# Optimization experiments

Measured on AMD Instinct MI355X. Metric: run time of the kernel, lower is better.

## Reference

```python
import jax, jax.numpy as jnp
import numpy as np

F = 128; K = 64; SR_CUT = 10.0
NB = 5; NRI = 3; NRA = 2; NRO = 1
N_ATOMS = 10000; N_PAIRS = 320000


def act(x):
    # shifted softplus: softplus(x) - log(2)
    return jax.nn.softplus(x) - jnp.log(2.0).astype(x.dtype)


def residual(x, W1, b1, W2, b2):
    # PhysNet residual: x + dense2(dense1(act(x))) with activation on dense1
    h = act(act(x) @ W1 + b1)
    return x + h @ W2 + b2


def cutoff_fn(D):
    x = D / SR_CUT
    x3 = x * x * x; x4 = x3 * x; x5 = x4 * x
    return jnp.where(x < 1.0, 1.0 - 6.0 * x5 + 15.0 * x4 - 10.0 * x3, 0.0)


def setup_inputs() -> dict:
    key = jax.random.key(0)
    ks = jax.random.split(key, 24)

    def nrm(k, shape, s=0.05):
        return (jax.random.normal(k, shape) * s).astype(jnp.float32)

    inp = {}
    inp["Z"] = jax.random.randint(ks[0], (N_ATOMS,), 1, 95)
    inp["R"] = (jax.random.normal(ks[1], (N_ATOMS, 3)) * 3.0).astype(jnp.float32)
    inp["idx_i"] = jax.random.randint(ks[2], (N_PAIRS,), 0, N_ATOMS)
    inp["idx_j"] = jax.random.randint(ks[3], (N_PAIRS,), 0, N_ATOMS)
    s3 = float(np.sqrt(3.0))
    inp["embeddings"] = jax.random.uniform(ks[4], (95, F), minval=-s3, maxval=s3).astype(jnp.float32)
    inp["rbf_centers"] = jnp.linspace(1.0, float(np.exp(-SR_CUT)), K).astype(jnp.float32)
    width = (0.5 / ((1.0 - float(np.exp(-SR_CUT))) / K)) ** 2
    inp["rbf_widths"] = jnp.full((K,), width, dtype=jnp.float32)
    inp["k2f_W"] = nrm(ks[5], (NB, K, F))
    inp["Wi"] = nrm(ks[6], (NB, F, F)); inp["bi"] = jnp.zeros((NB, F), jnp.float32)
    inp["Wj"] = nrm(ks[7], (NB, F, F)); inp["bj"] = jnp.zeros((NB, F), jnp.float32)
    inp["ri_W1"] = nrm(ks[8], (NB, NRI, F, F)); inp["ri_b1"] = jnp.zeros((NB, NRI, F), jnp.float32)
    inp["ri_W2"] = nrm(ks[9], (NB, NRI, F, F)); inp["ri_b2"] = jnp.zeros((NB, NRI, F), jnp.float32)
    inp["dW"] = nrm(ks[10], (NB, F, F)); inp["db"] = jnp.zeros((NB, F), jnp.float32)
    inp["u"] = jnp.ones((NB, F), jnp.float32)
    inp["ra_W1"] = nrm(ks[11], (NB, NRA, F, F)); inp["ra_b1"] = jnp.zeros((NB, NRA, F), jnp.float32)
    inp["ra_W2"] = nrm(ks[12], (NB, NRA, F, F)); inp["ra_b2"] = jnp.zeros((NB, NRA, F), jnp.float32)
    inp["ro_W1"] = nrm(ks[13], (NB, NRO, F, F)); inp["ro_b1"] = jnp.zeros((NB, NRO, F), jnp.float32)
    inp["ro_W2"] = nrm(ks[14], (NB, NRO, F, F)); inp["ro_b2"] = jnp.zeros((NB, NRO, F), jnp.float32)
    inp["out_W"] = nrm(ks[15], (NB, F, 2))
    inp["Escale"] = jnp.ones((95,), jnp.float32); inp["Eshift"] = jnp.zeros((95,), jnp.float32)
    inp["Qscale"] = jnp.ones((95,), jnp.float32); inp["Qshift"] = jnp.zeros((95,), jnp.float32)
    return inp


def reference(Z, R, idx_i, idx_j, embeddings, rbf_centers, rbf_widths, k2f_W, Wi, bi, Wj, bj,
              ri_W1, ri_b1, ri_W2, ri_b2, dW, db, u, ra_W1, ra_b1, ra_W2, ra_b2,
              ro_W1, ro_b1, ro_W2, ro_b2, out_W, Escale, Eshift, Qscale, Qshift):
    N = R.shape[0]
    # gather-based interatomic distances: gather -> sub -> sumsq -> relu -> sqrt
    dR = R[idx_i] - R[idx_j]                                   # [P,3]
    Dij = jnp.sqrt(jax.nn.relu(jnp.sum(dR * dR, axis=-1)))     # [P]
    # RBF expansion with smooth cutoff
    rbf = cutoff_fn(Dij)[:, None] * jnp.exp(-rbf_widths * (jnp.exp(-Dij)[:, None] - rbf_centers) ** 2)  # [P,K]
    x = embeddings[Z]                                          # [N,F]
    Ea = jnp.zeros((N,), x.dtype)
    Qa = jnp.zeros((N,), x.dtype)
    nhloss = jnp.zeros((), x.dtype)
    last2 = None
    for b in range(NB):
        # --- interaction layer ---
        g = rbf @ k2f_W[b]                                     # [P,F]
        xa = act(x)
        xi = act(xa @ Wi[b] + bi[b])                           # [N,F]
        xj_feat = act(xa @ Wj[b] + bj[b])                      # [N,F]
        msg = g * xj_feat[idx_j]                               # [P,F] gather + modulate
        m = xi + jax.ops.segment_sum(msg, idx_i, num_segments=N)
        for l in range(NRI):
            m = residual(m, ri_W1[b, l], ri_b1[b, l], ri_W2[b, l], ri_b2[b, l])
        m = act(m)
        x = u[b] * x + m @ dW[b] + db[b]
        for l in range(NRA):
            x = residual(x, ra_W1[b, l], ra_b1[b, l], ra_W2[b, l], ra_b2[b, l])
        # --- output block ---
        o = x
        for l in range(NRO):
            o = residual(o, ro_W1[b, l], ro_b1[b, l], ro_W2[b, l], ro_b2[b, l])
        out = act(o) @ out_W[b]                                # [N,2] -> (Ea, Qa)
        Ea = Ea + out[:, 0]
        Qa = Qa + out[:, 1]
        out2 = out * out
        if b > 0:
            nhloss = nhloss + jnp.mean(out2 / (out2 + last2 + 1e-7))
        last2 = out2
    Ea = Escale[Z] * Ea + Eshift[Z]
    Qa = Qscale[Z] * Qa + Qshift[Z]
    return Ea, Qa, Dij, nhloss
```

## Files before the change

kernel.cpp:

```cpp
#include <hip/hip_runtime.h>

typedef __attribute__((ext_vector_type(8))) short bfrag;
typedef __attribute__((ext_vector_type(4))) float ffrag;

__device__ __forceinline__ unsigned short f2b(float f){
  unsigned int u = __float_as_uint(f);
  return (unsigned short)((u + 0x7FFFu + ((u >> 16) & 1u)) >> 16);
}
__device__ __forceinline__ float actf(float v){
  float e = __builtin_amdgcn_exp2f(-fabsf(v)*1.44269504088896341f);
  return fmaxf(v, 0.f) + __builtin_amdgcn_logf(1.f + e)*0.69314718055994531f - 0.69314718055994531f;
}

__global__ __launch_bounds__(256) void k_zero(float* p, int n){
  int i = blockIdx.x*256 + threadIdx.x;
  if (i < n) p[i] = 0.f;
}

__global__ __launch_bounds__(256) void k_dij_count(
    const float* __restrict__ R, const int* __restrict__ idx_i, const int* __restrict__ idx_j,
    float* __restrict__ DijF, float* __restrict__ Dout, int* __restrict__ counts, int P){
  int p = blockIdx.x*256 + threadIdx.x;
  if (p >= P) return;
  int i = idx_i[p], j = idx_j[p];
  float dx = R[i*3+0] - R[j*3+0];
  float dy = R[i*3+1] - R[j*3+1];
  float dz = R[i*3+2] - R[j*3+2];
  float D = sqrtf(fmaxf(dx*dx + dy*dy + dz*dz, 0.f));
  DijF[p] = D;
  Dout[p] = D;
  atomicAdd(&counts[i], 1);
}

__global__ __launch_bounds__(256) void k_scanA(const int* __restrict__ counts,
    int* __restrict__ locEx, int* __restrict__ bsum, int N){
  __shared__ int buf[256];
  int tid = threadIdx.x, idx = blockIdx.x*256 + tid;
  int v = (idx < N) ? counts[idx] : 0;
  buf[tid] = v;
  __syncthreads();
  for (int off = 1; off < 256; off <<= 1){
    int t = (tid >= off) ? buf[tid-off] : 0;
    __syncthreads();
    buf[tid] += t;
    __syncthreads();
  }
  if (idx < N) locEx[idx] = buf[tid] - v;
  if (tid == 255) bsum[blockIdx.x] = buf[255];
}
__global__ __launch_bounds__(64) void k_scanB(int* __restrict__ bsum,
    int* __restrict__ boff, int nb){
  if (threadIdx.x == 0){
    int acc = 0;
    for (int i = 0; i < nb; ++i){ boff[i] = acc; acc += bsum[i]; }
    boff[nb] = acc;
  }
}
__global__ __launch_bounds__(256) void k_scanC(const int* __restrict__ locEx,
    const int* __restrict__ boff, int* __restrict__ starts, int* __restrict__ cursor,
    int N, int nb){
  int idx = blockIdx.x*256 + threadIdx.x;
  if (idx < N){
    int s = locEx[idx] + boff[blockIdx.x];
    starts[idx] = s; cursor[idx] = s;
  }
  if (idx == 0) starts[N] = boff[nb];
}

__global__ __launch_bounds__(256) void k_scatter(const int* __restrict__ idx_i,
    const int* __restrict__ idx_j, const float* __restrict__ DijF,
    int* __restrict__ cursor, int* __restrict__ i_s, int* __restrict__ j_s,
    float* __restrict__ D_s, int P){
  int p = blockIdx.x*256 + threadIdx.x;
  if (p >= P) return;
  int i = idx_i[p];
  int pos = atomicAdd(&cursor[i], 1);
  i_s[pos] = i;
  j_s[pos] = idx_j[p];
  D_s[pos] = DijF[p];
}

__global__ __launch_bounds__(256) void k_rbf(
    const float* __restrict__ D_s, const float* __restrict__ cent, const float* __restrict__ wid,
    unsigned short* __restrict__ rbf_s, int P){
  int gid = blockIdx.x*256 + threadIdx.x;
  if (gid >= P*64) return;
  int t = gid >> 6, k = gid & 63;
  float D = D_s[t];
  float xc = D * 0.1f;
  float cut = 0.f;
  if (xc < 1.f){
    float x3 = xc*xc*xc, x4 = x3*xc, x5 = x4*xc;
    cut = 1.f - 6.f*x5 + 15.f*x4 - 10.f*x3;
  }
  float tt = expf(-D) - cent[k];
  rbf_s[gid] = f2b(cut * expf(-wid[k]*tt*tt));
}

__global__ __launch_bounds__(256) void k_prep(const float* __restrict__ k2f,
    unsigned short* __restrict__ k2fP){
  int gid = blockIdx.x*256 + threadIdx.x;
  if (gid >= 5120) return;
  int l = gid & 63, fr = (gid >> 6) & 15, b = gid >> 10;
  int tile = fr >> 1, kh = fr & 1;
  const float* src = k2f + (size_t)b*64*128;
  int n = tile*16 + (l & 15);
  int kbase = kh*32 + (l >> 4)*8;
  ushort4 o0, o1;
  o0.x = f2b(src[(kbase+0)*128+n]); o0.y = f2b(src[(kbase+1)*128+n]);
  o0.z = f2b(src[(kbase+2)*128+n]); o0.w = f2b(src[(kbase+3)*128+n]);
  o1.x = f2b(src[(kbase+4)*128+n]); o1.y = f2b(src[(kbase+5)*128+n]);
  o1.z = f2b(src[(kbase+6)*128+n]); o1.w = f2b(src[(kbase+7)*128+n]);
  ushort4* dst = (ushort4*)(k2fP + (size_t)gid*8);
  dst[0] = o0; dst[1] = o1;
}

__global__ __launch_bounds__(256) void k_prepAll(
    const float* __restrict__ riW1, const float* __restrict__ riW2,
    const float* __restrict__ dW,   const float* __restrict__ raW1,
    const float* __restrict__ raW2, const float* __restrict__ roW1,
    const float* __restrict__ roW2, const float* __restrict__ Wi,
    const float* __restrict__ Wj,   unsigned short* __restrict__ WBall){
  int gid = blockIdx.x*256 + threadIdx.x;
  if (gid >= 75*2048) return;
  int i = gid >> 11, r = gid & 2047;
  const float* S;
  int slot;
  if (i < 15)      { S = riW1 + (size_t)i*16384;      slot = (i/3)*15 + 2*(i%3); }
  else if (i < 30) { int j=i-15; S = riW2 + (size_t)j*16384; slot = (j/3)*15 + 2*(j%3) + 1; }
  else if (i < 35) { int j=i-30; S = dW   + (size_t)j*16384; slot = j*15 + 6; }
  else if (i < 45) { int j=i-35; S = raW1 + (size_t)j*16384; slot = (j/2)*15 + 7 + 2*(j%2); }
  else if (i < 55) { int j=i-45; S = raW2 + (size_t)j*16384; slot = (j/2)*15 + 8 + 2*(j%2); }
  else if (i < 60) { int j=i-55; S = roW1 + (size_t)j*16384; slot = j*15 + 11; }
  else if (i < 65) { int j=i-60; S = roW2 + (size_t)j*16384; slot = j*15 + 12; }
  else if (i < 70) { int j=i-65; S = Wi   + (size_t)j*16384; slot = ((j==0)?4:(j-1))*15 + 13; }
  else             { int j=i-70; S = Wj   + (size_t)j*16384; slot = ((j==0)?4:(j-1))*15 + 14; }
  int fr = r >> 6, l = r & 63;
  int T = fr >> 2, k0 = fr & 3;
  int n = T*16 + (l & 15);
  int kbase = k0*32 + (l >> 4)*8;
  unsigned short* D = WBall + ((size_t)slot*2048 + r)*8;
  ushort4 o0, o1;
  o0.x=f2b(S[(kbase+0)*128+n]); o0.y=f2b(S[(kbase+1)*128+n]);
  o0.z=f2b(S[(kbase+2)*128+n]); o0.w=f2b(S[(kbase+3)*128+n]);
  o1.x=f2b(S[(kbase+4)*128+n]); o1.y=f2b(S[(kbase+5)*128+n]);
  o1.z=f2b(S[(kbase+6)*128+n]); o1.w=f2b(S[(kbase+7)*128+n]);
  ((ushort4*)D)[0]=o0; ((ushort4*)D)[1]=o1;
}

__global__ __launch_bounds__(256) void k_prepO(const float* __restrict__ outW,
    unsigned short* __restrict__ outWB){
  int gid = blockIdx.x*256 + threadIdx.x;
  if (gid >= 5*256) return;
  int b = gid >> 8, r = gid & 255;
  int l = r & 63;
  int col = l & 15;
  int k0 = r >> 6;
  int kbase = k0*32 + (l >> 4)*8;
  ushort4 o0 = {0,0,0,0}, o1 = {0,0,0,0};
  if (col < 2){
    const float* S = outW + (size_t)b*256;
    o0.x=f2b(S[(kbase+0)*2+col]); o0.y=f2b(S[(kbase+1)*2+col]);
    o0.z=f2b(S[(kbase+2)*2+col]); o0.w=f2b(S[(kbase+3)*2+col]);
    o1.x=f2b(S[(kbase+4)*2+col]); o1.y=f2b(S[(kbase+5)*2+col]);
    o1.z=f2b(S[(kbase+6)*2+col]); o1.w=f2b(S[(kbase+7)*2+col]);
  }
  unsigned short* D = outWB + ((size_t)b*256 + r)*8;
  ((ushort4*)D)[0]=o0; ((ushort4*)D)[1]=o1;
}

__device__ __forceinline__ void mmtile(const unsigned short* tile,
    const unsigned short* __restrict__ WB, int w, int l, ffrag C[4]){
  int m = l & 15, q = l >> 4;
  bfrag A[4];
  #pragma unroll
  for (int k0 = 0; k0 < 4; ++k0)
    A[k0] = *(const bfrag*)(tile + m*136 + k0*32 + q*8);
  #pragma unroll
  for (int tt = 0; tt < 4; ++tt){
    ffrag c = {0.f,0.f,0.f,0.f};
    const bfrag* bp = (const bfrag*)(WB + (((w*4+tt)*4)*64 + l)*8);
    #pragma unroll
    for (int k0 = 0; k0 < 4; ++k0)
      c = __builtin_amdgcn_mfma_f32_16x16x32_bf16(A[k0], bp[k0*64], c, 0, 0, 0);
    C[tt] = c;
  }
}

__device__ __forceinline__ void loadB8(const unsigned short* __restrict__ WB,
    int w, int l, bfrag* B){
  #pragma unroll
  for (int tt = 0; tt < 2; ++tt)
    #pragma unroll
    for (int k0 = 0; k0 < 4; ++k0)
      B[tt*4+k0] = *(const bfrag*)(WB + ((size_t)((((w*2+tt)*4)+k0)*64 + l))*8);
}
__device__ __forceinline__ void mmB(const unsigned short* tile, const bfrag* B,
    int l, ffrag C[2]){
  int m = l & 15, q = l >> 4;
  bfrag A[4];
  #pragma unroll
  for (int k0 = 0; k0 < 4; ++k0)
    A[k0] = *(const bfrag*)(tile + m*136 + k0*32 + q*8);
  #pragma unroll
  for (int tt = 0; tt < 2; ++tt){
    ffrag c = {0.f,0.f,0.f,0.f};
    #pragma unroll
    for (int k0 = 0; k0 < 4; ++k0)
      c = __builtin_amdgcn_mfma_f32_16x16x32_bf16(A[k0], B[tt*4+k0], c, 0, 0, 0);
    C[tt] = c;
  }
}

__global__ __launch_bounds__(128) void k_phase1m(
    const int* __restrict__ Z, const float* __restrict__ emb,
    const unsigned short* __restrict__ WB45,
    const float* __restrict__ bi0, const float* __restrict__ bj0,
    float* __restrict__ x_g, float* __restrict__ m_g, float* __restrict__ xjb_g, int N){
  __shared__ unsigned short tile[16*136];
  int tid = threadIdx.x, w = tid >> 6, l = tid & 63;
  int m = l & 15, q = l >> 4, rbase = blockIdx.x*16;
  #pragma unroll
  for (int r = 0; r < 4; ++r){
    int row = rbase + q*4 + r;
    int z = Z[row];
    #pragma unroll
    for (int tt = 0; tt < 4; ++tt){
      int c = (w*4+tt)*16 + m;
      float v = emb[(size_t)z*128 + c];
      x_g[(size_t)row*128 + c] = v;
      tile[(q*4+r)*136 + c] = f2b(actf(v));
    }
  }
  __syncthreads();
  ffrag C[4];
  mmtile(tile, WB45 + 13*16384, w, l, C);
  #pragma unroll
  for (int tt = 0; tt < 4; ++tt){
    int c = (w*4+tt)*16 + m;
    float bb = bi0[c];
    #pragma unroll
    for (int r = 0; r < 4; ++r)
      m_g[(size_t)(rbase + q*4 + r)*128 + c] = actf(C[tt][r] + bb);
  }
  mmtile(tile, WB45 + 14*16384, w, l, C);
  #pragma unroll
  for (int tt = 0; tt < 4; ++tt){
    int c = (w*4+tt)*16 + m;
    float bb = bj0[c];
    #pragma unroll
    for (int r = 0; r < 4; ++r)
      xjb_g[(size_t)(rbase + q*4 + r)*128 + c] = actf(C[tt][r] + bb);
  }
}

__global__ __launch_bounds__(256) void k_pairmsg2(
    const unsigned short* __restrict__ rbf_s, const unsigned short* __restrict__ k2fP,
    const int* __restrict__ i_s, const int* __restrict__ j_s,
    const float* __restrict__ xj, float* __restrict__ m_g, int P){
  __shared__ float G[4][16*130];
  int tid = threadIdx.x, w = tid >> 6, l = tid & 63;
  float* Gw = &G[w][0];
  bfrag B[16];
  #pragma unroll
  for (int t = 0; t < 8; ++t){
    #pragma unroll
    for (int kh = 0; kh < 2; ++kh)
      B[t*2+kh] = *(const bfrag*)(k2fP + (size_t)((t*2+kh)*64 + l)*8);
  }
  int wstart = (blockIdx.x*4 + w)*128;
  if (wstart >= P) return;
  int row16 = l & 15, quad = l >> 4;
  float a0 = 0.f, a1 = 0.f;
  int iCur = -1;
  bfrag A0 = *(const bfrag*)(rbf_s + (size_t)(wstart + row16)*64 + quad*8);
  bfrag A1 = *(const bfrag*)(rbf_s + (size_t)(wstart + row16)*64 + 32 + quad*8);
  int4 iv[4], jv[4];
  #pragma unroll
  for (int g = 0; g < 4; ++g){
    iv[g] = *(const int4*)(i_s + wstart + g*4);
    jv[g] = *(const int4*)(j_s + wstart + g*4);
  }
  #pragma unroll 1
  for (int bi2 = 0; bi2 < 8; ++bi2){
    int bt = wstart + bi2*16;
    const int* ip = (const int*)iv;
    const int* jp = (const int*)jv;
    float2 xv[16];
    #pragma unroll
    for (int k = 0; k < 16; ++k)
      xv[k] = *(const float2*)(xj + (size_t)jp[k]*128 + 2*l);
    #pragma unroll
    for (int t = 0; t < 8; ++t){
      ffrag C = {0.f,0.f,0.f,0.f};
      C = __builtin_amdgcn_mfma_f32_16x16x32_bf16(A0, B[t*2],   C, 0, 0, 0);
      C = __builtin_amdgcn_mfma_f32_16x16x32_bf16(A1, B[t*2+1], C, 0, 0, 0);
      #pragma unroll
      for (int r = 0; r < 4; ++r)
        Gw[(quad*4+r)*130 + t*16 + row16] = C[r];
    }
    bfrag nA0, nA1;
    int4 niv[4], njv[4];
    if (bi2 < 7){
      int btn = bt + 16;
      nA0 = *(const bfrag*)(rbf_s + (size_t)(btn + row16)*64 + quad*8);
      nA1 = *(const bfrag*)(rbf_s + (size_t)(btn + row16)*64 + 32 + quad*8);
      #pragma unroll
      for (int g = 0; g < 4; ++g){
        niv[g] = *(const int4*)(i_s + btn + g*4);
        njv[g] = *(const int4*)(j_s + btn + g*4);
      }
    }
    #pragma unroll
    for (int k = 0; k < 16; ++k){
      int i = ip[k];
      if (i != iCur){
        if (iCur >= 0){
          unsafeAtomicAdd(&m_g[(size_t)iCur*128 + 2*l],     a0);
          unsafeAtomicAdd(&m_g[(size_t)iCur*128 + 2*l + 1], a1);
        }
        iCur = i; a0 = 0.f; a1 = 0.f;
      }
      float g0 = Gw[k*130 + 2*l], g1 = Gw[k*130 + 2*l + 1];
      a0 = fmaf(g0, xv[k].x, a0);
      a1 = fmaf(g1, xv[k].y, a1);
    }
    if (bi2 < 7){
      A0 = nA0; A1 = nA1;
      #pragma unroll
      for (int g = 0; g < 4; ++g){ iv[g] = niv[g]; jv[g] = njv[g]; }
    }
  }
  if (iCur >= 0){
    unsafeAtomicAdd(&m_g[(size_t)iCur*128 + 2*l],     a0);
    unsafeAtomicAdd(&m_g[(size_t)iCur*128 + 2*l + 1], a1);
  }
}

template<int HASNEXT, int NH>
__global__ __launch_bounds__(256) void k_phase2m(
    float* __restrict__ m_g, float* __restrict__ x_g, float* __restrict__ xjb_g,
    const unsigned short* __restrict__ WBb,
    const float* __restrict__ rib1, const float* __restrict__ rib2,
    const float* __restrict__ db, const float* __restrict__ u,
    const float* __restrict__ rab1, const float* __restrict__ rab2,
    const float* __restrict__ rob1, const float* __restrict__ rob2,
    const float* __restrict__ biN, const float* __restrict__ bjN,
    const unsigned short* __restrict__ outWBb,
    float* __restrict__ Ea, float* __restrict__ Qa,
    float* __restrict__ last2, float* __restrict__ nh, int N){
  __shared__ unsigned short tiles[2][16*136];
  __shared__ float biasS[16*128];
  int tid = threadIdx.x, w = tid >> 6, l = tid & 63;
  int m = l & 15, q = l >> 4, rbase = blockIdx.x*16;
  ffrag mC[2], xC[2], C[2];
  int cur = 0;
  const int nst = HASNEXT ? 15 : 13;
  const int slotSeq[15] = {0,1,2,3,4,5,6,7,8,9,10,
                           HASNEXT?13:11, HASNEXT?14:12, 11, 12};
  bfrag Bb[2][8];
  loadB8(WBb + (size_t)slotSeq[0]*16384, w, l, Bb[0]);

  if (tid < 128){
    biasS[0*128+tid]  = rib1[tid];
    biasS[1*128+tid]  = rib1[128+tid];
    biasS[2*128+tid]  = rib1[256+tid];
    biasS[3*128+tid]  = rib2[tid];
    biasS[4*128+tid]  = rib2[128+tid];
    biasS[5*128+tid]  = rib2[256+tid];
    biasS[6*128+tid]  = db[tid];
    biasS[7*128+tid]  = u[tid];
    biasS[8*128+tid]  = rab1[tid];
    biasS[9*128+tid]  = rab1[128+tid];
    biasS[10*128+tid] = rab2[tid];
    biasS[11*128+tid] = rab2[128+tid];
    biasS[12*128+tid] = rob1[tid];
    biasS[13*128+tid] = rob2[tid];
    biasS[14*128+tid] = biN[tid];
    biasS[15*128+tid] = bjN[tid];
  }
  float xrow[2][4];
  #pragma unroll
  for (int tt = 0; tt < 2; ++tt){
    int c = (w*2+tt)*16 + m;
    #pragma unroll
    for (int r = 0; r < 4; ++r)
      xrow[tt][r] = x_g[(size_t)(rbase + q*4 + r)*128 + c];
  }
  #pragma unroll
  for (int tt = 0; tt < 2; ++tt){
    int c = (w*2+tt)*16 + m;
    #pragma unroll
    for (int r = 0; r < 4; ++r){
      float v = m_g[(size_t)(rbase + q*4 + r)*128 + c];
      mC[tt][r] = v;
      tiles[0][(q*4+r)*136 + c] = f2b(actf(v));
    }
  }
  #pragma unroll
  for (int s = 0; s < nst; ++s){
    __syncthreads();
    if (s+1 < nst) loadB8(WBb + (size_t)slotSeq[s+1]*16384, w, l, Bb[(s+1)&1]);
    mmB(tiles[cur], Bb[s&1], l, C);
    if (HASNEXT && s == 11){
      #pragma unroll
      for (int tt = 0; tt < 2; ++tt){
        int c = (w*2+tt)*16 + m;
        float bb = biasS[14*128 + c];
        #pragma unroll
        for (int r = 0; r < 4; ++r)
          m_g[(size_t)(rbase + q*4 + r)*128 + c] = actf(C[tt][r] + bb);
      }
    } else if (HASNEXT && s == 12){
      #pragma unroll
      for (int tt = 0; tt < 2; ++tt){
        int c = (w*2+tt)*16 + m;
        float bb = biasS[15*128 + c];
        #pragma unroll
        for (int r = 0; r < 4; ++r)
          xjb_g[(size_t)(rbase + q*4 + r)*128 + c] = actf(C[tt][r] + bb);
      }
    } else if (s == 6){
      #pragma unroll
      for (int tt = 0; tt < 2; ++tt){
        int c = (w*2+tt)*16 + m;
        float uu = biasS[7*128 + c], bb = biasS[6*128 + c];
        #pragma unroll
        for (int r = 0; r < 4; ++r){
          float nv = uu*xrow[tt][r] + C[tt][r] + bb;
          xC[tt][r] = nv;
          tiles[1-cur][(q*4+r)*136 + c] = f2b(actf(nv));
        }
      }
      cur ^= 1;
    } else if (s == 1 || s == 3 || s == 5){
      #pragma unroll
      for (int tt = 0; tt < 2; ++tt){
        int c = (w*2+tt)*16 + m;
        float bb = biasS[(3 + (s>>1))*128 + c];
        #pragma unroll
        for (int r = 0; r < 4; ++r){
          float nv = mC[tt][r] + C[tt][r] + bb;
          mC[tt][r] = nv;
          tiles[1-cur][(q*4+r)*136 + c] = f2b(actf(nv));
        }
      }
      cur ^= 1;
    } else if (s == 8 || s == 10){
      #pragma unroll
      for (int tt = 0; tt < 2; ++tt){
        int c = (w*2+tt)*16 + m;
        float bb = biasS[(10 + ((s-8)>>1))*128 + c];
        #pragma unroll
        for (int r = 0; r < 4; ++r){
          float nv = xC[tt][r] + C[tt][r] + bb;
          xC[tt][r] = nv;
          tiles[1-cur][(q*4+r)*136 + c] = f2b(actf(nv));
          if (HASNEXT && s == 10)
            x_g[(size_t)(rbase + q*4 + r)*128 + c] = nv;
        }
      }
      cur ^= 1;
    } else if ((HASNEXT && s == 14) || (!HASNEXT && s == 12)){
      #pragma unroll
      for (int tt = 0; tt < 2; ++tt){
        int c = (w*2+tt)*16 + m;
        float bb = biasS[13*128 + c];
        #pragma unroll
        for (int r = 0; r < 4; ++r){
          float ov = xC[tt][r] + C[tt][r] + bb;
          tiles[1-cur][(q*4+r)*136 + c] = f2b(actf(ov));
        }
      }
      cur ^= 1;
    } else {
      int bidx = (s==0)?0:(s==2)?1:(s==4)?2:(s==7)?8:(s==9)?9:12;
      #pragma unroll
      for (int tt = 0; tt < 2; ++tt){
        int c = (w*2+tt)*16 + m;
        float bb = biasS[bidx*128 + c];
        #pragma unroll
        for (int r = 0; r < 4; ++r)
          tiles[1-cur][(q*4+r)*136 + c] = f2b(actf(C[tt][r] + bb));
      }
      cur ^= 1;
    }
  }
  __syncthreads();
  if (w == 0){
    bfrag A[4];
    #pragma unroll
    for (int k0 = 0; k0 < 4; ++k0)
      A[k0] = *(const bfrag*)(&tiles[cur][0] + m*136 + k0*32 + q*8);
    ffrag Ch = {0.f,0.f,0.f,0.f};
    #pragma unroll
    for (int k0 = 0; k0 < 4; ++k0){
      bfrag B = *(const bfrag*)(outWBb + (size_t)(k0*64 + l)*8);
      Ch = __builtin_amdgcn_mfma_f32_16x16x32_bf16(A[k0], B, Ch, 0, 0, 0);
    }
    int col = m;
    if (col < 2){
      float tp = 0.f;
      #pragma unroll
      for (int r = 0; r < 4; ++r){
        int row = rbase + q*4 + r;
        float val = Ch[r];
        if (col == 0) Ea[row] += val; else Qa[row] += val;
        float sq = val*val;
        if (NH){
          float lastv = last2[row*2 + col];
          tp += sq/(sq + lastv + 1e-7f);
        }
        last2[row*2 + col] = sq;
      }
      if (NH) unsafeAtomicAdd(nh, tp);
    }
  }
}

__global__ __launch_bounds__(256) void k_final(
    const int* __restrict__ Z, const float* __restrict__ Ea, const float* __restrict__ Qa,
    const float* __restrict__ Es, const float* __restrict__ Eh,
    const float* __restrict__ Qs, const float* __restrict__ Qh,
    const float* __restrict__ nh, float* __restrict__ out, int N, int P){
  int n = blockIdx.x*256 + threadIdx.x;
  if (n < N){
    int z = Z[n];
    out[n]   = Es[z]*Ea[n] + Eh[z];
    out[N+n] = Qs[z]*Qa[n] + Qh[z];
  }
  if (blockIdx.x == 0 && threadIdx.x == 0)
    out[(size_t)2*N + P] = nh[0] / (2.f * (float)N);
}

extern "C" void kernel_launch(void* const* d_in, const int* in_sizes, int n_in,
                              void* d_out, int out_size, void* d_ws, size_t ws_size,
                              hipStream_t stream){
  const int N = in_sizes[0];
  const int P = in_sizes[2];
  const int F = 128;

  const int* Z      = (const int*)d_in[0];
  const float* R    = (const float*)d_in[1];
  const int* idx_i  = (const int*)d_in[2];
  const int* idx_j  = (const int*)d_in[3];
  const float* emb  = (const float*)d_in[4];
  const float* cent = (const float*)d_in[5];
  const float* wid  = (const float*)d_in[6];
  const float* k2f  = (const float*)d_in[7];
  const float* Wi   = (const float*)d_in[8];  const float* bi   = (const float*)d_in[9];
  const float* Wj   = (const float*)d_in[10]; const float* bj   = (const float*)d_in[11];
  const float* riW1 = (const float*)d_in[12]; const float* rib1 = (const float*)d_in[13];
  const float* riW2 = (const float*)d_in[14]; const float* rib2 = (const float*)d_in[15];
  const float* dWp  = (const float*)d_in[16]; const float* dbp  = (const float*)d_in[17];
  const float* u    = (const float*)d_in[18];
  const float* raW1 = (const float*)d_in[19]; const float* rab1 = (const float*)d_in[20];
  const float* raW2 = (const float*)d_in[21]; const float* rab2 = (const float*)d_in[22];
  const float* roW1 = (const float*)d_in[23]; const float* rob1 = (const float*)d_in[24];
  const float* roW2 = (const float*)d_in[25]; const float* rob2 = (const float*)d_in[26];
  const float* outW = (const float*)d_in[27];
  const float* Es   = (const float*)d_in[28]; const float* Eh   = (const float*)d_in[29];
  const float* Qs   = (const float*)d_in[30]; const float* Qh   = (const float*)d_in[31];

  char* ws = (char*)d_ws;
  size_t off = 0;
  float* DijF  = (float*)(ws + off); off += (size_t)P*4;
  float* D_s   = (float*)(ws + off); off += (size_t)P*4;
  int*   i_s   = (int*)  (ws + off); off += (size_t)P*4;
  int*   j_s   = (int*)  (ws + off); off += (size_t)P*4;
  unsigned short* rbf_s = (unsigned short*)(ws + off); off += (size_t)P*64*2;
  unsigned short* k2fP  = (unsigned short*)(ws + off); off += (size_t)5*16*64*8*2;
  unsigned short* WBall = (unsigned short*)(ws + off); off += (size_t)75*16384*2;
  unsigned short* outWB = (unsigned short*)(ws + off); off += (size_t)5*2048*2;
  float* x     = (float*)(ws + off); off += (size_t)N*F*4;
  float* xjb   = (float*)(ws + off); off += (size_t)N*F*4;
  float* m     = (float*)(ws + off); off += (size_t)N*F*4;
  float* last2 = (float*)(ws + off); off += (size_t)N*2*4;
  float* Ea    = (float*)(ws + off); off += (size_t)N*4;
  float* Qa    = (float*)(ws + off); off += (size_t)N*4;
  float* nh    = (float*)(ws + off); off += 256;
  int*   counts= (int*)  (ws + off); off += (size_t)N*4;
  int*   starts= (int*)  (ws + off); off += (size_t)(N+1)*4;
  int*   cursor= (int*)  (ws + off); off += (size_t)N*4;
  int*   locEx = (int*)  (ws + off); off += (size_t)N*4;
  int*   bsum  = (int*)  (ws + off); off += 64*4;
  int*   boff  = (int*)  (ws + off); off += 68*4;

  float* outF = (float*)d_out;
  float* Dout = outF + (size_t)2*N;

  const int nb = (N + 255)/256;
  const int nzero = 3*N + 64;
  k_zero<<<dim3((nzero+255)/256), dim3(256), 0, stream>>>(Ea, nzero);
  k_dij_count<<<dim3((P+255)/256), dim3(256), 0, stream>>>(R, idx_i, idx_j, DijF, Dout, counts, P);
  k_scanA<<<dim3(nb), dim3(256), 0, stream>>>(counts, locEx, bsum, N);
  k_scanB<<<dim3(1), dim3(64), 0, stream>>>(bsum, boff, nb);
  k_scanC<<<dim3(nb), dim3(256), 0, stream>>>(locEx, boff, starts, cursor, N, nb);
  k_scatter<<<dim3((P+255)/256), dim3(256), 0, stream>>>(idx_i, idx_j, DijF, cursor, i_s, j_s, D_s, P);
  k_rbf<<<dim3((P*64+255)/256), dim3(256), 0, stream>>>(D_s, cent, wid, rbf_s, P);
  k_prep<<<dim3(20), dim3(256), 0, stream>>>(k2f, k2fP);
  k_prepAll<<<dim3((75*2048+255)/256), dim3(256), 0, stream>>>(riW1, riW2, dWp, raW1, raW2,
                                                               roW1, roW2, Wi, Wj, WBall);
  k_prepO<<<dim3(5), dim3(256), 0, stream>>>(outW, outWB);

  const int G16 = (N + 15)/16;
  k_phase1m<<<dim3(G16), dim3(128), 0, stream>>>(Z, emb, WBall + (size_t)4*15*16384,
                                                 bi, bj, x, m, xjb, N);

  const int pmg = (P + 511)/512;
  for (int b = 0; b < 5; ++b){
    k_pairmsg2<<<dim3(pmg), dim3(256), 0, stream>>>(rbf_s, k2fP + (size_t)b*16*64*8,
                                                    i_s, j_s, xjb, m, P);
    const unsigned short* WBb = WBall + (size_t)b*15*16384;
    const float* a_rib1 = rib1 + (size_t)b*3*F;
    const float* a_rib2 = rib2 + (size_t)b*3*F;
    const float* a_db   = dbp  + (size_t)b*F;
    const float* a_u    = u    + (size_t)b*F;
    const float* a_rab1 = rab1 + (size_t)b*2*F;
    const float* a_rab2 = rab2 + (size_t)b*2*F;
    const float* a_rob1 = rob1 + (size_t)b*F;
    const float* a_rob2 = rob2 + (size_t)b*F;
    int bn = (b < 4) ? (b+1) : 0;
    const float* a_biN = bi + (size_t)bn*F;
    const float* a_bjN = bj + (size_t)bn*F;
    const unsigned short* oWB = outWB + (size_t)b*2048;
    if (b == 0){
      k_phase2m<1,0><<<dim3(G16), dim3(256), 0, stream>>>(m, x, xjb, WBb,
        a_rib1, a_rib2, a_db, a_u, a_rab1, a_rab2, a_rob1, a_rob2,
        a_biN, a_bjN, oWB, Ea, Qa, last2, nh, N);
    } else if (b < 4){
      k_phase2m<1,1><<<dim3(G16), dim3(256), 0, stream>>>(m, x, xjb, WBb,
        a_rib1, a_rib2, a_db, a_u, a_rab1, a_rab2, a_rob1, a_rob2,
        a_biN, a_bjN, oWB, Ea, Qa, last2, nh, N);
    } else {
      k_phase2m<0,1><<<dim3(G16), dim3(256), 0, stream>>>(m, x, xjb, WBb,
        a_rib1, a_rib2, a_db, a_u, a_rab1, a_rab2, a_rob1, a_rob2,
        a_biN, a_bjN, oWB, Ea, Qa, last2, nh, N);
    }
  }
  k_final<<<dim3((N+255)/256), dim3(256), 0, stream>>>(Z, Ea, Qa, Es, Eh, Qs, Qh, nh, outF, N, P);
}
```

Before: 518.8 us.

## Merge scan and prep kernels, vectorize RBF, widen phase2 blocks to 32 rows

```diff
diff --git a/kernel.cpp b/kernel.cpp
--- a/kernel.cpp
+++ b/kernel.cpp
@@ -32,39 +32,42 @@
   atomicAdd(&counts[i], 1);
 }
 
-__global__ __launch_bounds__(256) void k_scanA(const int* __restrict__ counts,
-    int* __restrict__ locEx, int* __restrict__ bsum, int N){
-  __shared__ int buf[256];
-  int tid = threadIdx.x, idx = blockIdx.x*256 + tid;
-  int v = (idx < N) ? counts[idx] : 0;
-  buf[tid] = v;
+__global__ __launch_bounds__(1024) void k_scan(const int* __restrict__ counts,
+    int* __restrict__ cursor, int N){
+  __shared__ int wsum[16];
+  int tid = threadIdx.x;
+  int CH = (N + 1023) >> 10;
+  int base = tid * CH;
+  int s = 0;
+  for (int i = 0; i < CH; ++i){
+    int idx = base + i;
+    s += (idx < N) ? counts[idx] : 0;
+  }
+  int lane = tid & 63, w = tid >> 6;
+  int v = s;
+  #pragma unroll
+  for (int off = 1; off < 64; off <<= 1){
+    int t = __shfl_up(v, off, 64);
+    if (lane >= off) v += t;
+  }
+  if (lane == 63) wsum[w] = v;
   __syncthreads();
-  for (int off = 1; off < 256; off <<= 1){
-    int t = (tid >= off) ? buf[tid-off] : 0;
-    __syncthreads();
-    buf[tid] += t;
-    __syncthreads();
-  }
-  if (idx < N) locEx[idx] = buf[tid] - v;
-  if (tid == 255) bsum[blockIdx.x] = buf[255];
-}
-__global__ __launch_bounds__(64) void k_scanB(int* __restrict__ bsum,
-    int* __restrict__ boff, int nb){
-  if (threadIdx.x == 0){
-    int acc = 0;
-    for (int i = 0; i < nb; ++i){ boff[i] = acc; acc += bsum[i]; }
-    boff[nb] = acc;
-  }
-}
-__global__ __launch_bounds__(256) void k_scanC(const int* __restrict__ locEx,
-    const int* __restrict__ boff, int* __restrict__ starts, int* __restrict__ cursor,
-    int N, int nb){
-  int idx = blockIdx.x*256 + threadIdx.x;
-  if (idx < N){
-    int s = locEx[idx] + boff[blockIdx.x];
-    starts[idx] = s; cursor[idx] = s;
-  }
-  if (idx == 0) starts[N] = boff[nb];
+  if (tid < 16){
+    int t = wsum[tid];
+    int vv = t;
+    #pragma unroll
+    for (int off = 1; off < 16; off <<= 1){
+      int u = __shfl_up(vv, off, 64);
+      if (tid >= off) vv += u;
+    }
+    wsum[tid] = vv - t;
+  }
+  __syncthreads();
+  int run = (v - s) + wsum[w];
+  for (int i = 0; i < CH; ++i){
+    int idx = base + i;
+    if (idx < N){ cursor[idx] = run; run += counts[idx]; }
+  }
 }
 
 __global__ __launch_bounds__(256) void k_scatter(const int* __restrict__ idx_i,
@@ -84,8 +87,8 @@
     const float* __restrict__ D_s, const float* __restrict__ cent, const float* __restrict__ wid,
     unsigned short* __restrict__ rbf_s, int P){
   int gid = blockIdx.x*256 + threadIdx.x;
-  if (gid >= P*64) return;
-  int t = gid >> 6, k = gid & 63;
+  if (gid >= P*8) return;
+  int t = gid >> 3, kg = gid & 7;
   float D = D_s[t];
   float xc = D * 0.1f;
   float cut = 0.f;
@@ -93,26 +96,16 @@
     float x3 = xc*xc*xc, x4 = x3*xc, x5 = x4*xc;
     cut = 1.f - 6.f*x5 + 15.f*x4 - 10.f*x3;
   }
-  float tt = expf(-D) - cent[k];
-  rbf_s[gid] = f2b(cut * expf(-wid[k]*tt*tt));
-}
-
-__global__ __launch_bounds__(256) void k_prep(const float* __restrict__ k2f,
-    unsigned short* __restrict__ k2fP){
-  int gid = blockIdx.x*256 + threadIdx.x;
-  if (gid >= 5120) return;
-  int l = gid & 63, fr = (gid >> 6) & 15, b = gid >> 10;
-  int tile = fr >> 1, kh = fr & 1;
-  const float* src = k2f + (size_t)b*64*128;
-  int n = tile*16 + (l & 15);
-  int kbase = kh*32 + (l >> 4)*8;
-  ushort4 o0, o1;
-  o0.x = f2b(src[(kbase+0)*128+n]); o0.y = f2b(src[(kbase+1)*128+n]);
-  o0.z = f2b(src[(kbase+2)*128+n]); o0.w = f2b(src[(kbase+3)*128+n]);
-  o1.x = f2b(src[(kbase+4)*128+n]); o1.y = f2b(src[(kbase+5)*128+n]);
-  o1.z = f2b(src[(kbase+6)*128+n]); o1.w = f2b(src[(kbase+7)*128+n]);
-  ushort4* dst = (ushort4*)(k2fP + (size_t)gid*8);
-  dst[0] = o0; dst[1] = o1;
+  float eD = __builtin_amdgcn_exp2f(-D*1.44269504088896341f);
+  bfrag o;
+  #pragma unroll
+  for (int i = 0; i < 8; ++i){
+    int k = kg*8 + i;
+    float tt = eD - cent[k];
+    float v = cut * __builtin_amdgcn_exp2f(-wid[k]*tt*tt*1.44269504088896341f);
+    o[i] = (short)f2b(v);
+  }
+  *(bfrag*)(rbf_s + (size_t)gid*8) = o;
 }
 
 __global__ __launch_bounds__(256) void k_prepAll(
@@ -120,53 +113,67 @@
     const float* __restrict__ dW,   const float* __restrict__ raW1,
     const float* __restrict__ raW2, const float* __restrict__ roW1,
     const float* __restrict__ roW2, const float* __restrict__ Wi,
-    const float* __restrict__ Wj,   unsigned short* __restrict__ WBall){
-  int gid = blockIdx.x*256 + threadIdx.x;
-  if (gid >= 75*2048) return;
-  int i = gid >> 11, r = gid & 2047;
-  const float* S;
-  int slot;
-  if (i < 15)      { S = riW1 + (size_t)i*16384;      slot = (i/3)*15 + 2*(i%3); }
-  else if (i < 30) { int j=i-15; S = riW2 + (size_t)j*16384; slot = (j/3)*15 + 2*(j%3) + 1; }
-  else if (i < 35) { int j=i-30; S = dW   + (size_t)j*16384; slot = j*15 + 6; }
-  else if (i < 45) { int j=i-35; S = raW1 + (size_t)j*16384; slot = (j/2)*15 + 7 + 2*(j%2); }
-  else if (i < 55) { int j=i-45; S = raW2 + (size_t)j*16384; slot = (j/2)*15 + 8 + 2*(j%2); }
-  else if (i < 60) { int j=i-55; S = roW1 + (size_t)j*16384; slot = j*15 + 11; }
-  else if (i < 65) { int j=i-60; S = roW2 + (size_t)j*16384; slot = j*15 + 12; }
-  else if (i < 70) { int j=i-65; S = Wi   + (size_t)j*16384; slot = ((j==0)?4:(j-1))*15 + 13; }
-  else             { int j=i-70; S = Wj   + (size_t)j*16384; slot = ((j==0)?4:(j-1))*15 + 14; }
-  int fr = r >> 6, l = r & 63;
-  int T = fr >> 2, k0 = fr & 3;
-  int n = T*16 + (l & 15);
-  int kbase = k0*32 + (l >> 4)*8;
-  unsigned short* D = WBall + ((size_t)slot*2048 + r)*8;
-  ushort4 o0, o1;
-  o0.x=f2b(S[(kbase+0)*128+n]); o0.y=f2b(S[(kbase+1)*128+n]);
-  o0.z=f2b(S[(kbase+2)*128+n]); o0.w=f2b(S[(kbase+3)*128+n]);
-  o1.x=f2b(S[(kbase+4)*128+n]); o1.y=f2b(S[(kbase+5)*128+n]);
-  o1.z=f2b(S[(kbase+6)*128+n]); o1.w=f2b(S[(kbase+7)*128+n]);
-  ((ushort4*)D)[0]=o0; ((ushort4*)D)[1]=o1;
-}
-
-__global__ __launch_bounds__(256) void k_prepO(const float* __restrict__ outW,
+    const float* __restrict__ Wj,   const float* __restrict__ k2f,
+    const float* __restrict__ outW,
+    unsigned short* __restrict__ WBall, unsigned short* __restrict__ k2fP,
     unsigned short* __restrict__ outWB){
   int gid = blockIdx.x*256 + threadIdx.x;
-  if (gid >= 5*256) return;
-  int b = gid >> 8, r = gid & 255;
-  int l = r & 63;
-  int col = l & 15;
-  int k0 = r >> 6;
-  int kbase = k0*32 + (l >> 4)*8;
-  ushort4 o0 = {0,0,0,0}, o1 = {0,0,0,0};
-  if (col < 2){
-    const float* S = outW + (size_t)b*256;
-    o0.x=f2b(S[(kbase+0)*2+col]); o0.y=f2b(S[(kbase+1)*2+col]);
-    o0.z=f2b(S[(kbase+2)*2+col]); o0.w=f2b(S[(kbase+3)*2+col]);
-    o1.x=f2b(S[(kbase+4)*2+col]); o1.y=f2b(S[(kbase+5)*2+col]);
-    o1.z=f2b(S[(kbase+6)*2+col]); o1.w=f2b(S[(kbase+7)*2+col]);
-  }
-  unsigned short* D = outWB + ((size_t)b*256 + r)*8;
-  ((ushort4*)D)[0]=o0; ((ushort4*)D)[1]=o1;
+  if (gid < 75*2048){
+    int i = gid >> 11, r = gid & 2047;
+    const float* S;
+    int slot;
+    if (i < 15)      { S = riW1 + (size_t)i*16384;      slot = (i/3)*15 + 2*(i%3); }
+    else if (i < 30) { int j=i-15; S = riW2 + (size_t)j*16384; slot = (j/3)*15 + 2*(j%3) + 1; }
+    else if (i < 35) { int j=i-30; S = dW   + (size_t)j*16384; slot = j*15 + 6; }
+    else if (i < 45) { int j=i-35; S = raW1 + (size_t)j*16384; slot = (j/2)*15 + 7 + 2*(j%2); }
+    else if (i < 55) { int j=i-45; S = raW2 + (size_t)j*16384; slot = (j/2)*15 + 8 + 2*(j%2); }
+    else if (i < 60) { int j=i-55; S = roW1 + (size_t)j*16384; slot = j*15 + 11; }
+    else if (i < 65) { int j=i-60; S = roW2 + (size_t)j*16384; slot = j*15 + 12; }
+    else if (i < 70) { int j=i-65; S = Wi   + (size_t)j*16384; slot = ((j==0)?4:(j-1))*15 + 13; }
+    else             { int j=i-70; S = Wj   + (size_t)j*16384; slot = ((j==0)?4:(j-1))*15 + 14; }
+    int fr = r >> 6, l = r & 63;
+    int T = fr >> 2, k0 = fr & 3;
+    int n = T*16 + (l & 15);
+    int kbase = k0*32 + (l >> 4)*8;
+    unsigned short* D = WBall + ((size_t)slot*2048 + r)*8;
+    ushort4 o0, o1;
+    o0.x=f2b(S[(kbase+0)*128+n]); o0.y=f2b(S[(kbase+1)*128+n]);
+    o0.z=f2b(S[(kbase+2)*128+n]); o0.w=f2b(S[(kbase+3)*128+n]);
+    o1.x=f2b(S[(kbase+4)*128+n]); o1.y=f2b(S[(kbase+5)*128+n]);
+    o1.z=f2b(S[(kbase+6)*128+n]); o1.w=f2b(S[(kbase+7)*128+n]);
+    ((ushort4*)D)[0]=o0; ((ushort4*)D)[1]=o1;
+  } else if (gid < 75*2048 + 5120){
+    int g = gid - 75*2048;
+    int l = g & 63, fr = (g >> 6) & 15, b = g >> 10;
+    int tile = fr >> 1, kh = fr & 1;
+    const float* src = k2f + (size_t)b*64*128;
+    int n = tile*16 + (l & 15);
+    int kbase = kh*32 + (l >> 4)*8;
+    ushort4 o0, o1;
+    o0.x = f2b(src[(kbase+0)*128+n]); o0.y = f2b(src[(kbase+1)*128+n]);
+    o0.z = f2b(src[(kbase+2)*128+n]); o0.w = f2b(src[(kbase+3)*128+n]);
+    o1.x = f2b(src[(kbase+4)*128+n]); o1.y = f2b(src[(kbase+5)*128+n]);
+    o1.z = f2b(src[(kbase+6)*128+n]); o1.w = f2b(src[(kbase+7)*128+n]);
+    ushort4* dst = (ushort4*)(k2fP + (size_t)g*8);
+    dst[0] = o0; dst[1] = o1;
+  } else if (gid < 75*2048 + 5120 + 1280){
+    int g = gid - (75*2048 + 5120);
+    int b = g >> 8, r = g & 255;
+    int l = r & 63;
+    int col = l & 15;
+    int k0 = r >> 6;
+    int kbase = k0*32 + (l >> 4)*8;
+    ushort4 o0 = {0,0,0,0}, o1 = {0,0,0,0};
+    if (col < 2){
+      const float* S = outW + (size_t)b*256;
+      o0.x=f2b(S[(kbase+0)*2+col]); o0.y=f2b(S[(kbase+1)*2+col]);
+      o0.z=f2b(S[(kbase+2)*2+col]); o0.w=f2b(S[(kbase+3)*2+col]);
+      o1.x=f2b(S[(kbase+4)*2+col]); o1.y=f2b(S[(kbase+5)*2+col]);
+      o1.z=f2b(S[(kbase+6)*2+col]); o1.w=f2b(S[(kbase+7)*2+col]);
+    }
+    unsigned short* D = outWB + ((size_t)b*256 + r)*8;
+    ((ushort4*)D)[0]=o0; ((ushort4*)D)[1]=o1;
+  }
 }
 
 __device__ __forceinline__ void mmtile(const unsigned short* tile,
@@ -183,31 +190,6 @@
     #pragma unroll
     for (int k0 = 0; k0 < 4; ++k0)
       c = __builtin_amdgcn_mfma_f32_16x16x32_bf16(A[k0], bp[k0*64], c, 0, 0, 0);
-    C[tt] = c;
-  }
-}
-
-__device__ __forceinline__ void loadB8(const unsigned short* __restrict__ WB,
-    int w, int l, bfrag* B){
-  #pragma unroll
-  for (int tt = 0; tt < 2; ++tt)
-    #pragma unroll
-    for (int k0 = 0; k0 < 4; ++k0)
-      B[tt*4+k0] = *(const bfrag*)(WB + ((size_t)((((w*2+tt)*4)+k0)*64 + l))*8);
-}
-__device__ __forceinline__ void mmB(const unsigned short* tile, const bfrag* B,
-    int l, ffrag C[2]){
-  int m = l & 15, q = l >> 4;
-  bfrag A[4];
-  #pragma unroll
-  for (int k0 = 0; k0 < 4; ++k0)
-    A[k0] = *(const bfrag*)(tile + m*136 + k0*32 + q*8);
-  #pragma unroll
-  for (int tt = 0; tt < 2; ++tt){
-    ffrag c = {0.f,0.f,0.f,0.f};
-    #pragma unroll
-    for (int k0 = 0; k0 < 4; ++k0)
-      c = __builtin_amdgcn_mfma_f32_16x16x32_bf16(A[k0], B[tt*4+k0], c, 0, 0, 0);
     C[tt] = c;
   }
 }
@@ -338,7 +320,7 @@
 }
 
 template<int HASNEXT, int NH>
-__global__ __launch_bounds__(256) void k_phase2m(
+__global__ __launch_bounds__(512) void k_phase2m(
     float* __restrict__ m_g, float* __restrict__ x_g, float* __restrict__ xjb_g,
     const unsigned short* __restrict__ WBb,
     const float* __restrict__ rib1, const float* __restrict__ rib2,
@@ -349,17 +331,21 @@
     const unsigned short* __restrict__ outWBb,
     float* __restrict__ Ea, float* __restrict__ Qa,
     float* __restrict__ last2, float* __restrict__ nh, int N){
-  __shared__ unsigned short tiles[2][16*136];
+  __shared__ unsigned short tiles[2][2][16*136];
   __shared__ float biasS[16*128];
   int tid = threadIdx.x, w = tid >> 6, l = tid & 63;
-  int m = l & 15, q = l >> 4, rbase = blockIdx.x*16;
+  int m = l & 15, q = l >> 4, rbase = blockIdx.x*32;
+  int c = w*16 + m;
   ffrag mC[2], xC[2], C[2];
+  float xrow[2][4];
   int cur = 0;
   const int nst = HASNEXT ? 15 : 13;
   const int slotSeq[15] = {0,1,2,3,4,5,6,7,8,9,10,
                            HASNEXT?13:11, HASNEXT?14:12, 11, 12};
-  bfrag Bb[2][8];
-  loadB8(WBb + (size_t)slotSeq[0]*16384, w, l, Bb[0]);
+  bfrag Bb[2][4];
+  #pragma unroll
+  for (int k0 = 0; k0 < 4; ++k0)
+    Bb[0][k0] = *(const bfrag*)(WBb + (size_t)slotSeq[0]*16384 + (size_t)((w*4+k0)*64 + l)*8);
 
   if (tid < 128){
     biasS[0*128+tid]  = rib1[tid];
@@ -379,119 +365,120 @@
     biasS[14*128+tid] = biN[tid];
     biasS[15*128+tid] = bjN[tid];
   }
-  float xrow[2][4];
-  #pragma unroll
-  for (int tt = 0; tt < 2; ++tt){
-    int c = (w*2+tt)*16 + m;
-    #pragma unroll
-    for (int r = 0; r < 4; ++r)
-      xrow[tt][r] = x_g[(size_t)(rbase + q*4 + r)*128 + c];
-  }
-  #pragma unroll
-  for (int tt = 0; tt < 2; ++tt){
-    int c = (w*2+tt)*16 + m;
+  #pragma unroll
+  for (int h = 0; h < 2; ++h){
     #pragma unroll
     for (int r = 0; r < 4; ++r){
-      float v = m_g[(size_t)(rbase + q*4 + r)*128 + c];
-      mC[tt][r] = v;
-      tiles[0][(q*4+r)*136 + c] = f2b(actf(v));
-    }
-  }
-  #pragma unroll
+      int row = rbase + h*16 + q*4 + r;
+      int rs = row < N ? row : N-1;
+      xrow[h][r] = x_g[(size_t)rs*128 + c];
+      float v = m_g[(size_t)rs*128 + c];
+      mC[h][r] = v;
+      tiles[h][0][(q*4+r)*136 + c] = f2b(actf(v));
+    }
+  }
+  #pragma unroll 2
   for (int s = 0; s < nst; ++s){
     __syncthreads();
-    if (s+1 < nst) loadB8(WBb + (size_t)slotSeq[s+1]*16384, w, l, Bb[(s+1)&1]);
-    mmB(tiles[cur], Bb[s&1], l, C);
+    if (s+1 < nst){
+      #pragma unroll
+      for (int k0 = 0; k0 < 4; ++k0)
+        Bb[(s+1)&1][k0] = *(const bfrag*)(WBb + (size_t)slotSeq[s+1]*16384 + (size_t)((w*4+k0)*64 + l)*8);
+    }
+    #pragma unroll
+    for (int h = 0; h < 2; ++h){
+      const unsigned short* tp = &tiles[h][cur][0];
+      ffrag cc = {0.f,0.f,0.f,0.f};
+      #pragma unroll
+      for (int k0 = 0; k0 < 4; ++k0){
+        bfrag A = *(const bfrag*)(tp + m*136 + k0*32 + q*8);
+        cc = __builtin_amdgcn_mfma_f32_16x16x32_bf16(A, Bb[s&1][k0], cc, 0, 0, 0);
+      }
+      C[h] = cc;
+    }
     if (HASNEXT && s == 11){
-      #pragma unroll
-      for (int tt = 0; tt < 2; ++tt){
-        int c = (w*2+tt)*16 + m;
-        float bb = biasS[14*128 + c];
-        #pragma unroll
-        for (int r = 0; r < 4; ++r)
-          m_g[(size_t)(rbase + q*4 + r)*128 + c] = actf(C[tt][r] + bb);
-      }
-    } else if (HASNEXT && s == 12){
-      #pragma unroll
-      for (int tt = 0; tt < 2; ++tt){
-        int c = (w*2+tt)*16 + m;
-        float bb = biasS[15*128 + c];
-        #pragma unroll
-        for (int r = 0; r < 4; ++r)
-          xjb_g[(size_t)(rbase + q*4 + r)*128 + c] = actf(C[tt][r] + bb);
-      }
-    } else if (s == 6){
-      #pragma unroll
-      for (int tt = 0; tt < 2; ++tt){
-        int c = (w*2+tt)*16 + m;
-        float uu = biasS[7*128 + c], bb = biasS[6*128 + c];
+      float bb = biasS[14*128 + c];
+      #pragma unroll
+      for (int h = 0; h < 2; ++h)
         #pragma unroll
         for (int r = 0; r < 4; ++r){
-          float nv = uu*xrow[tt][r] + C[tt][r] + bb;
-          xC[tt][r] = nv;
-          tiles[1-cur][(q*4+r)*136 + c] = f2b(actf(nv));
-        }
-      }
+          int row = rbase + h*16 + q*4 + r;
+          if (row < N) m_g[(size_t)row*128 + c] = actf(C[h][r] + bb);
+        }
+    } else if (HASNEXT && s == 12){
+      float bb = biasS[15*128 + c];
+      #pragma unroll
+      for (int h = 0; h < 2; ++h)
+        #pragma unroll
+        for (int r = 0; r < 4; ++r){
+          int row = rbase + h*16 + q*4 + r;
+          if (row < N) xjb_g[(size_t)row*128 + c] = actf(C[h][r] + bb);
+        }
+    } else if (s == 6){
+      float uu = biasS[7*128 + c], bb = biasS[6*128 + c];
+      #pragma unroll
+      for (int h = 0; h < 2; ++h)
+        #pragma unroll
+        for (int r = 0; r < 4; ++r){
+          float nv = uu*xrow[h][r] + C[h][r] + bb;
+          xC[h][r] = nv;
+          tiles[h][1-cur][(q*4+r)*136 + c] = f2b(actf(nv));
+        }
       cur ^= 1;
     } else if (s == 1 || s == 3 || s == 5){
-      #pragma unroll
-      for (int tt = 0; tt < 2; ++tt){
-        int c = (w*2+tt)*16 + m;
-        float bb = biasS[(3 + (s>>1))*128 + c];
+      float bb = biasS[(3 + (s>>1))*128 + c];
+      #pragma unroll
+      for (int h = 0; h < 2; ++h)
         #pragma unroll
         for (int r = 0; r < 4; ++r){
-          float nv = mC[tt][r] + C[tt][r] + bb;
-          mC[tt][r] = nv;
-          tiles[1-cur][(q*4+r)*136 + c] = f2b(actf(nv));
-        }
-      }
+          float nv = mC[h][r] + C[h][r] + bb;
+          mC[h][r] = nv;
+          tiles[h][1-cur][(q*4+r)*136 + c] = f2b(actf(nv));
+        }
       cur ^= 1;
     } else if (s == 8 || s == 10){
-      #pragma unroll
-      for (int tt = 0; tt < 2; ++tt){
-        int c = (w*2+tt)*16 + m;
-        float bb = biasS[(10 + ((s-8)>>1))*128 + c];
+      float bb = biasS[(10 + ((s-8)>>1))*128 + c];
+      #pragma unroll
+      for (int h = 0; h < 2; ++h)
         #pragma unroll
         for (int r = 0; r < 4; ++r){
-          float nv = xC[tt][r] + C[tt][r] + bb;
-          xC[tt][r] = nv;
-          tiles[1-cur][(q*4+r)*136 + c] = f2b(actf(nv));
-          if (HASNEXT && s == 10)
-            x_g[(size_t)(rbase + q*4 + r)*128 + c] = nv;
-        }
-      }
+          float nv = xC[h][r] + C[h][r] + bb;
+          xC[h][r] = nv;
+          tiles[h][1-cur][(q*4+r)*136 + c] = f2b(actf(nv));
+          if (HASNEXT && s == 10){
+            int row = rbase + h*16 + q*4 + r;
+            if (row < N) x_g[(size_t)row*128 + c] = nv;
+          }
+        }
       cur ^= 1;
     } else if ((HASNEXT && s == 14) || (!HASNEXT && s == 12)){
-      #pragma unroll
-      for (int tt = 0; tt < 2; ++tt){
-        int c = (w*2+tt)*16 + m;
-        float bb = biasS[13*128 + c];
+      float bb = biasS[13*128 + c];
+      #pragma unroll
+      for (int h = 0; h < 2; ++h)
         #pragma unroll
         for (int r = 0; r < 4; ++r){
-          float ov = xC[tt][r] + C[tt][r] + bb;
-          tiles[1-cur][(q*4+r)*136 + c] = f2b(actf(ov));
-        }
-      }
+          float ov = xC[h][r] + C[h][r] + bb;
+          tiles[h][1-cur][(q*4+r)*136 + c] = f2b(actf(ov));
+        }
       cur ^= 1;
     } else {
       int bidx = (s==0)?0:(s==2)?1:(s==4)?2:(s==7)?8:(s==9)?9:12;
-      #pragma unroll
-      for (int tt = 0; tt < 2; ++tt){
-        int c = (w*2+tt)*16 + m;
-        float bb = biasS[bidx*128 + c];
+      float bb = biasS[bidx*128 + c];
+      #pragma unroll
+      for (int h = 0; h < 2; ++h)
         #pragma unroll
         for (int r = 0; r < 4; ++r)
-          tiles[1-cur][(q*4+r)*136 + c] = f2b(actf(C[tt][r] + bb));
-      }
+          tiles[h][1-cur][(q*4+r)*136 + c] = f2b(actf(C[h][r] + bb));
       cur ^= 1;
     }
   }
   __syncthreads();
-  if (w == 0){
+  if (w < 2){
+    const unsigned short* tp = &tiles[w][cur][0];
     bfrag A[4];
     #pragma unroll
     for (int k0 = 0; k0 < 4; ++k0)
-      A[k0] = *(const bfrag*)(&tiles[cur][0] + m*136 + k0*32 + q*8);
+      A[k0] = *(const bfrag*)(tp + m*136 + k0*32 + q*8);
     ffrag Ch = {0.f,0.f,0.f,0.f};
     #pragma unroll
     for (int k0 = 0; k0 < 4; ++k0){
@@ -500,20 +487,26 @@
     }
     int col = m;
     if (col < 2){
-      float tp = 0.f;
+      float tpa = 0.f;
       #pragma unroll
       for (int r = 0; r < 4; ++r){
-        int row = rbase + q*4 + r;
-        float val = Ch[r];
-        if (col == 0) Ea[row] += val; else Qa[row] += val;
-        float sq = val*val;
-        if (NH){
-          float lastv = last2[row*2 + col];
-          tp += sq/(sq + lastv + 1e-7f);
-        }
-        last2[row*2 + col] = sq;
+        int row = rbase + w*16 + q*4 + r;
+        if (row < N){
+          float val = Ch[r];
+          if (NH){
+            if (col == 0) Ea[row] += val; else Qa[row] += val;
+          } else {
+            if (col == 0) Ea[row]  = val; else Qa[row]  = val;
+          }
+          float sq = val*val;
+          if (NH){
+            float lastv = last2[row*2 + col];
+            tpa += sq/(sq + lastv + 1e-7f);
+          }
+          last2[row*2 + col] = sq;
+        }
       }
-      if (NH) unsafeAtomicAdd(nh, tp);
+      if (NH) unsafeAtomicAdd(nh, tpa);
     }
   }
 }
@@ -580,34 +573,26 @@
   float* Qa    = (float*)(ws + off); off += (size_t)N*4;
   float* nh    = (float*)(ws + off); off += 256;
   int*   counts= (int*)  (ws + off); off += (size_t)N*4;
-  int*   starts= (int*)  (ws + off); off += (size_t)(N+1)*4;
   int*   cursor= (int*)  (ws + off); off += (size_t)N*4;
-  int*   locEx = (int*)  (ws + off); off += (size_t)N*4;
-  int*   bsum  = (int*)  (ws + off); off += 64*4;
-  int*   boff  = (int*)  (ws + off); off += 68*4;
 
   float* outF = (float*)d_out;
   float* Dout = outF + (size_t)2*N;
 
-  const int nb = (N + 255)/256;
-  const int nzero = 3*N + 64;
-  k_zero<<<dim3((nzero+255)/256), dim3(256), 0, stream>>>(Ea, nzero);
+  const int nzero = N + 64;
+  k_zero<<<dim3((nzero+255)/256), dim3(256), 0, stream>>>(nh, nzero);
   k_dij_count<<<dim3((P+255)/256), dim3(256), 0, stream>>>(R, idx_i, idx_j, DijF, Dout, counts, P);
-  k_scanA<<<dim3(nb), dim3(256), 0, stream>>>(counts, locEx, bsum, N);
-  k_scanB<<<dim3(1), dim3(64), 0, stream>>>(bsum, boff, nb);
-  k_scanC<<<dim3(nb), dim3(256), 0, stream>>>(locEx, boff, starts, cursor, N, nb);
+  k_scan<<<dim3(1), dim3(1024), 0, stream>>>(counts, cursor, N);
   k_scatter<<<dim3((P+255)/256), dim3(256), 0, stream>>>(idx_i, idx_j, DijF, cursor, i_s, j_s, D_s, P);
-  k_rbf<<<dim3((P*64+255)/256), dim3(256), 0, stream>>>(D_s, cent, wid, rbf_s, P);
-  k_prep<<<dim3(20), dim3(256), 0, stream>>>(k2f, k2fP);
-  k_prepAll<<<dim3((75*2048+255)/256), dim3(256), 0, stream>>>(riW1, riW2, dWp, raW1, raW2,
-                                                               roW1, roW2, Wi, Wj, WBall);
-  k_prepO<<<dim3(5), dim3(256), 0, stream>>>(outW, outWB);
+  k_rbf<<<dim3((P*8+255)/256), dim3(256), 0, stream>>>(D_s, cent, wid, rbf_s, P);
+  k_prepAll<<<dim3((75*2048 + 5120 + 1280 + 255)/256), dim3(256), 0, stream>>>(
+      riW1, riW2, dWp, raW1, raW2, roW1, roW2, Wi, Wj, k2f, outW, WBall, k2fP, outWB);
 
   const int G16 = (N + 15)/16;
   k_phase1m<<<dim3(G16), dim3(128), 0, stream>>>(Z, emb, WBall + (size_t)4*15*16384,
                                                  bi, bj, x, m, xjb, N);
 
   const int pmg = (P + 511)/512;
+  const int G32 = (N + 31)/32;
   for (int b = 0; b < 5; ++b){
     k_pairmsg2<<<dim3(pmg), dim3(256), 0, stream>>>(rbf_s, k2fP + (size_t)b*16*64*8,
                                                     i_s, j_s, xjb, m, P);
@@ -625,15 +610,15 @@
     const float* a_bjN = bj + (size_t)bn*F;
     const unsigned short* oWB = outWB + (size_t)b*2048;
     if (b == 0){
-      k_phase2m<1,0><<<dim3(G16), dim3(256), 0, stream>>>(m, x, xjb, WBb,
+      k_phase2m<1,0><<<dim3(G32), dim3(512), 0, stream>>>(m, x, xjb, WBb,
         a_rib1, a_rib2, a_db, a_u, a_rab1, a_rab2, a_rob1, a_rob2,
         a_biN, a_bjN, oWB, Ea, Qa, last2, nh, N);
     } else if (b < 4){
-      k_phase2m<1,1><<<dim3(G16), dim3(256), 0, stream>>>(m, x, xjb, WBb,
+      k_phase2m<1,1><<<dim3(G32), dim3(512), 0, stream>>>(m, x, xjb, WBb,
         a_rib1, a_rib2, a_db, a_u, a_rab1, a_rab2, a_rob1, a_rob2,
         a_biN, a_bjN, oWB, Ea, Qa, last2, nh, N);
     } else {
-      k_phase2m<0,1><<<dim3(G16), dim3(256), 0, stream>>>(m, x, xjb, WBb,
+      k_phase2m<0,1><<<dim3(G32), dim3(512), 0, stream>>>(m, x, xjb, WBb,
         a_rib1, a_rib2, a_db, a_u, a_rab1, a_rab2, a_rob1, a_rob2,
         a_biN, a_bjN, oWB, Ea, Qa, last2, nh, N);
     }
```

Measured after the change: 509.2 us. No clear change (-1.9%).
